# Performance work log

Measured on AMD Instinct MI355X. Metric: run time of the kernel, lower is better.

The kernel has to match this reference:

```python
import jax, jax.numpy as jnp
import numpy as np

N_NODES = 100000
N_EDGES = 1600000
IN_CH, HID, EMB = 128, 64, 32


def _glorot(key, shape):
    lim = np.sqrt(6.0 / (shape[0] + shape[1])).astype(np.float32)
    return jax.random.uniform(key, shape, jnp.float32, -lim, lim)


def setup_inputs() -> dict:
    key = jax.random.key(0)
    ks = jax.random.split(key, 5)
    x = jax.random.normal(ks[0], (N_NODES, IN_CH), dtype=jnp.float32)
    edges = jax.random.randint(ks[1], (2, N_EDGES), 0, N_NODES)
    W1 = _glorot(ks[2], (IN_CH, HID)); b1 = jnp.zeros((HID,), jnp.float32)
    W2 = _glorot(ks[3], (HID, EMB)); b2 = jnp.zeros((EMB,), jnp.float32)
    W3 = _glorot(ks[4], (HID, EMB)); b3 = jnp.zeros((EMB,), jnp.float32)
    return {"x": x, "edges": edges, "W1": W1, "b1": b1,
            "W2": W2, "b2": b2, "W3": W3, "b3": b3}


def reference(x, edges, W1, b1, W2, b2, W3, b3):
    N = x.shape[0]
    # GCNConv default: add self-loops, symmetric D^-1/2 A D^-1/2 normalization
    loop = jnp.arange(N, dtype=edges.dtype)
    src = jnp.concatenate([edges[0], loop])  # [E+N] message sources
    dst = jnp.concatenate([edges[1], loop])  # [E+N] message targets
    deg = jax.ops.segment_sum(jnp.ones_like(dst, dtype=x.dtype), dst, num_segments=N)
    dinv = jnp.where(deg > 0, jax.lax.rsqrt(deg), 0.0)
    norm = dinv[src] * dinv[dst]  # [E+N], cached across the three convs (cached=True)

    def gcn(h, W, b):
        h = h @ W                                  # [N, out]
        msg = h[src] * norm[:, None]               # gather + edge scale
        return jax.ops.segment_sum(msg, dst, num_segments=N) + b  # scatter-add

    h = jax.nn.relu(gcn(x, W1, b1))
    return gcn(h, W2, b2), gcn(h, W3, b3)
```

## Files before the change

### kernel.cpp

```cpp
#include <hip/hip_runtime.h>

#define NN 100000
#define NE 1600000
#define NB 391
#define CHUNK 4096
#define NCHUNK 391

typedef __attribute__((ext_vector_type(8))) short short8_t;
typedef __attribute__((ext_vector_type(4))) float float4_t;

__device__ inline unsigned short f2bf(float f) {
    unsigned int u = __float_as_uint(f);
    unsigned int r = u + 0x7fffu + ((u >> 16) & 1u);
    return (unsigned short)(r >> 16);
}
__device__ inline float bf_lo(unsigned int u) { return __uint_as_float(u << 16); }
__device__ inline float bf_hi(unsigned int u) { return __uint_as_float(u & 0xffff0000u); }

__global__ __launch_bounds__(256) void k_pre(const float* __restrict__ W1,
                                             unsigned short* __restrict__ wtb,
                                             int* __restrict__ bhist) {
    int f = blockIdx.x * 256 + threadIdx.x;
    int c = f >> 7, k = f & 127;
    wtb[f] = f2bf(W1[k * 64 + c]);
    if (f < NB) bhist[f] = 0;
}

__global__ __launch_bounds__(256) void k_hist(const int* __restrict__ dst,
                                              int* __restrict__ bhist) {
    __shared__ int lh[NB];
    int t = threadIdx.x;
    for (int i = t; i < NB; i += 256) lh[i] = 0;
    __syncthreads();
    for (int e = blockIdx.x * 256 + t; e < NE; e += 256 * 256)
        atomicAdd(&lh[dst[e] >> 8], 1);
    __syncthreads();
    for (int i = t; i < NB; i += 256)
        if (lh[i]) atomicAdd(&bhist[i], lh[i]);
}

__global__ __launch_bounds__(256) void k_scanb(const int* __restrict__ bhist,
                                               int* __restrict__ boff,
                                               int* __restrict__ bcur) {
    __shared__ int sh[256];
    int t = threadIdx.x;
    int base = t * 2;
    int v0 = (base + 0 < NB) ? bhist[base + 0] : 0;
    int v1 = (base + 1 < NB) ? bhist[base + 1] : 0;
    int tsum = v0 + v1;
    sh[t] = tsum;
    __syncthreads();
    for (int d = 1; d < 256; d <<= 1) {
        int x = (t >= d) ? sh[t - d] : 0;
        __syncthreads();
        sh[t] += x;
        __syncthreads();
    }
    int excl = sh[t] - tsum;
    if (base + 0 < NB) { boff[base + 0] = excl;      bcur[base + 0] = excl; }
    if (base + 1 < NB) { boff[base + 1] = excl + v0; bcur[base + 1] = excl + v0; }
    if (t == 255) boff[NB] = sh[255];
}

__global__ __launch_bounds__(512) void k_fuse(const float* __restrict__ x,
                                              const unsigned short* __restrict__ wtb,
                                              unsigned short* __restrict__ t1b,
                                              const int* __restrict__ src,
                                              const int* __restrict__ dst,
                                              int* __restrict__ bcur,
                                              unsigned int* __restrict__ pairs) {
    __shared__ __align__(16) unsigned char smem[52224];
    const int b = blockIdx.x;
    const int t = threadIdx.x;

    if ((b % 3) == 2) {
        int* lh    = (int*)smem;
        int* lbase = lh + NB;
        int e0 = (b / 3) * CHUNK;
        int e1 = min(e0 + CHUNK, NE);
        for (int i = t; i < NB; i += 512) lh[i] = 0;
        __syncthreads();
        for (int e = e0 + t; e < e1; e += 512)
            atomicAdd(&lh[dst[e] >> 8], 1);
        __syncthreads();
        int rot = (int)(((unsigned)(b / 3) * 97u) % NB);
        for (int i = t; i < NB; i += 512) {
            int ii = i + rot; if (ii >= NB) ii -= NB;
            int h = lh[ii];
            lbase[ii] = h ? atomicAdd(&bcur[ii], h) : 0;
        }
        __syncthreads();
        for (int i = t; i < NB; i += 512) lh[i] = 0;
        __syncthreads();
        for (int e = e0 + t; e < e1; e += 512) {
            int d = dst[e];
            int bk = d >> 8;
            int r = atomicAdd(&lh[bk], 1);
            pairs[lbase[bk] + r] = (unsigned int)src[e] | ((unsigned int)(d & 255) << 17);
        }
    } else {
        unsigned short* lx = (unsigned short*)smem;
        unsigned short* lw = (unsigned short*)(smem + 34816);
        const int tile = 2 * (b / 3) + (b % 3);
        const int row0 = tile * 128;
        const int nrows = min(128, NN - row0);

        #pragma unroll
        for (int i = 0; i < 8; ++i) {
            int f = t + i * 512;
            int r = f >> 5, c4 = f & 31;
            float4 v = make_float4(0.f, 0.f, 0.f, 0.f);
            if (r < nrows) v = ((const float4*)(x + (size_t)(row0 + r) * 128))[c4];
            ushort4 o;
            o.x = f2bf(v.x); o.y = f2bf(v.y); o.z = f2bf(v.z); o.w = f2bf(v.w);
            *(ushort4*)&lx[r * 136 + c4 * 4] = o;
        }
        #pragma unroll
        for (int i = 0; i < 2; ++i) {
            int f = t + i * 512;
            int c = f >> 4, c8 = f & 15;
            uint4 v = ((const uint4*)wtb)[f];
            *(uint4*)&lw[c * 136 + c8 * 8] = v;
        }
        __syncthreads();

        const int w = t >> 6, l = t & 63;
        const int m15 = l & 15, kg = l >> 4;
        const unsigned short* pa = &lx[(w * 16 + m15) * 136 + kg * 8];
        const unsigned short* pb = &lw[m15 * 136 + kg * 8];

        float4_t acc[4];
        #pragma unroll
        for (int cb = 0; cb < 4; ++cb) acc[cb] = (float4_t){0.f, 0.f, 0.f, 0.f};

        #pragma unroll
        for (int ks = 0; ks < 4; ++ks) {
            short8_t a = *(const short8_t*)(pa + ks * 32);
            #pragma unroll
            for (int cb = 0; cb < 4; ++cb) {
                short8_t bb = *(const short8_t*)(pb + cb * (16 * 136) + ks * 32);
                acc[cb] = __builtin_amdgcn_mfma_f32_16x16x32_bf16(a, bb, acc[cb], 0, 0, 0);
            }
        }

        #pragma unroll
        for (int r = 0; r < 4; ++r) {
            int lrow = w * 16 + kg * 4 + r;
            if (lrow < nrows) {
                size_t grow = (size_t)(row0 + lrow);
                #pragma unroll
                for (int cb = 0; cb < 4; ++cb)
                    t1b[grow * 64 + cb * 16 + m15] = f2bf(acc[cb][r]);
            }
        }
    }
}

__global__ __launch_bounds__(256) void k_fine(const unsigned int* __restrict__ pairs,
                                              const int* __restrict__ boff,
                                              int* __restrict__ csr_off,
                                              int* __restrict__ csr_src,
                                              float* __restrict__ dinv) {
    __shared__ int lcnt[256];
    __shared__ int sc[256];
    __shared__ int lofs[256];
    int t = threadIdx.x;
    int b = blockIdx.x;
    int n0 = b << 8;
    int nnode = min(256, NN - n0);
    int bO = boff[b], bE = boff[b + 1];

    lcnt[t] = 0;
    __syncthreads();
    for (int e = bO + t; e < bE; e += 256)
        atomicAdd(&lcnt[pairs[e] >> 17], 1);
    __syncthreads();
    sc[t] = lcnt[t];
    __syncthreads();
    for (int d = 1; d < 256; d <<= 1) {
        int x = (t >= d) ? sc[t - d] : 0;
        __syncthreads();
        sc[t] += x;
        __syncthreads();
    }
    {
        int excl = sc[t] - lcnt[t];
        lofs[t] = excl;
        if (t < nnode) {
            int n = n0 + t;
            csr_off[n] = bO + excl;
            dinv[n] = rsqrtf(1.0f + (float)lcnt[t]);
        }
        lcnt[t] = 0;
    }
    if (b == NB - 1 && t == 0) csr_off[NN] = NE;
    __syncthreads();
    for (int e = bO + t; e < bE; e += 256) {
        unsigned int w = pairs[e];
        int li = (int)(w >> 17);
        int r = atomicAdd(&lcnt[li], 1);
        csr_src[bO + lofs[li] + r] = (int)(w & 0x1FFFFu);
    }
}

__global__ __launch_bounds__(256) void k_gather8(const int* __restrict__ off,
                                                 const int* __restrict__ csr,
                                                 const float* __restrict__ dinv,
                                                 const unsigned short* __restrict__ hb,
                                                 const float* __restrict__ bias,
                                                 unsigned int* __restrict__ outp) {
    int idx = blockIdx.x * 256 + threadIdx.x;
    int n = idx >> 3;
    if (n >= NN) return;
    int c8 = idx & 7;
    const uint4* h4 = (const uint4*)hb;
    float dn = dinv[n];
    float a0[8], a1[8];
    {
        uint4 v = h4[(size_t)n * 8 + c8];
        a0[0] = dn * bf_lo(v.x); a0[1] = dn * bf_hi(v.x);
        a0[2] = dn * bf_lo(v.y); a0[3] = dn * bf_hi(v.y);
        a0[4] = dn * bf_lo(v.z); a0[5] = dn * bf_hi(v.z);
        a0[6] = dn * bf_lo(v.w); a0[7] = dn * bf_hi(v.w);
        #pragma unroll
        for (int j = 0; j < 8; ++j) a1[j] = 0.f;
    }
    int b = off[n], e = off[n + 1];
    int i = b;
    for (; i + 1 < e; i += 2) {
        int s0 = csr[i], s1 = csr[i + 1];
        float w0 = dinv[s0], w1 = dinv[s1];
        uint4 v0 = h4[(size_t)s0 * 8 + c8];
        uint4 v1 = h4[(size_t)s1 * 8 + c8];
        a0[0] += w0 * bf_lo(v0.x); a0[1] += w0 * bf_hi(v0.x);
        a0[2] += w0 * bf_lo(v0.y); a0[3] += w0 * bf_hi(v0.y);
        a0[4] += w0 * bf_lo(v0.z); a0[5] += w0 * bf_hi(v0.z);
        a0[6] += w0 * bf_lo(v0.w); a0[7] += w0 * bf_hi(v0.w);
        a1[0] += w1 * bf_lo(v1.x); a1[1] += w1 * bf_hi(v1.x);
        a1[2] += w1 * bf_lo(v1.y); a1[3] += w1 * bf_hi(v1.y);
        a1[4] += w1 * bf_lo(v1.z); a1[5] += w1 * bf_hi(v1.z);
        a1[6] += w1 * bf_lo(v1.w); a1[7] += w1 * bf_hi(v1.w);
    }
    if (i < e) {
        int s = csr[i];
        float w = dinv[s];
        uint4 v = h4[(size_t)s * 8 + c8];
        a0[0] += w * bf_lo(v.x); a0[1] += w * bf_hi(v.x);
        a0[2] += w * bf_lo(v.y); a0[3] += w * bf_hi(v.y);
        a0[4] += w * bf_lo(v.z); a0[5] += w * bf_hi(v.z);
        a0[6] += w * bf_lo(v.w); a0[7] += w * bf_hi(v.w);
    }
    float4 b0 = ((const float4*)bias)[c8 * 2];
    float4 b1v = ((const float4*)bias)[c8 * 2 + 1];
    float o[8];
    o[0] = dn * fmaxf(dn * (a0[0] + a1[0]) + b0.x, 0.f);
    o[1] = dn * fmaxf(dn * (a0[1] + a1[1]) + b0.y, 0.f);
    o[2] = dn * fmaxf(dn * (a0[2] + a1[2]) + b0.z, 0.f);
    o[3] = dn * fmaxf(dn * (a0[3] + a1[3]) + b0.w, 0.f);
    o[4] = dn * fmaxf(dn * (a0[4] + a1[4]) + b1v.x, 0.f);
    o[5] = dn * fmaxf(dn * (a0[5] + a1[5]) + b1v.y, 0.f);
    o[6] = dn * fmaxf(dn * (a0[6] + a1[6]) + b1v.z, 0.f);
    o[7] = dn * fmaxf(dn * (a0[7] + a1[7]) + b1v.w, 0.f);
    uint4 p;
    p.x = (unsigned int)f2bf(o[0]) | ((unsigned int)f2bf(o[1]) << 16);
    p.y = (unsigned int)f2bf(o[2]) | ((unsigned int)f2bf(o[3]) << 16);
    p.z = (unsigned int)f2bf(o[4]) | ((unsigned int)f2bf(o[5]) << 16);
    p.w = (unsigned int)f2bf(o[6]) | ((unsigned int)f2bf(o[7]) << 16);
    ((uint4*)outp)[(size_t)n * 8 + c8] = p;
}

__global__ __launch_bounds__(256) void k_gg2(const int* __restrict__ off,
                                             const int* __restrict__ csr,
                                             const float* __restrict__ dinv,
                                             const unsigned short* __restrict__ hb,
                                             const float* __restrict__ W2, const float* __restrict__ b2,
                                             const float* __restrict__ W3, const float* __restrict__ b3,
                                             float* __restrict__ out) {
    __shared__ float as_[32][72];
    __shared__ float wc[64 * 64];
    __shared__ float bc[64];
    const int t = threadIdx.x;
    const int row0 = blockIdx.x * 32;

    #pragma unroll
    for (int i = 0; i < 16; ++i) {
        int f = t + i * 256;
        int k = f >> 6, c = f & 63;
        wc[f] = (c < 32) ? W2[k * 32 + c] : W3[k * 32 + (c - 32)];
    }
    if (t < 64) bc[t] = (t < 32) ? b2[t] : b3[t - 32];

    {
        const int nl = t >> 3;
        const int n = row0 + nl;
        const int c8 = t & 7;
        const uint4* h4 = (const uint4*)hb;
        float dn = dinv[n];
        float acc[8];
        uint4 v = h4[(size_t)n * 8 + c8];
        acc[0] = bf_lo(v.x); acc[1] = bf_hi(v.x);
        acc[2] = bf_lo(v.y); acc[3] = bf_hi(v.y);
        acc[4] = bf_lo(v.z); acc[5] = bf_hi(v.z);
        acc[6] = bf_lo(v.w); acc[7] = bf_hi(v.w);
        int b = off[n], e = off[n + 1];
        for (int i = b; i < e; ++i) {
            int s = csr[i];
            uint4 u = h4[(size_t)s * 8 + c8];
            acc[0] += bf_lo(u.x); acc[1] += bf_hi(u.x);
            acc[2] += bf_lo(u.y); acc[3] += bf_hi(u.y);
            acc[4] += bf_lo(u.z); acc[5] += bf_hi(u.z);
            acc[6] += bf_lo(u.w); acc[7] += bf_hi(u.w);
        }
        float* dp = &as_[nl][c8 * 8];
        #pragma unroll
        for (int j = 0; j < 8; ++j) dp[j] = dn * acc[j];
    }
    __syncthreads();

    const int tc = t & 15;
    const int tr = t >> 4;
    float acc[2][4];
    #pragma unroll
    for (int i = 0; i < 2; ++i)
        #pragma unroll
        for (int j = 0; j < 4; ++j) acc[i][j] = 0.f;

    #pragma unroll 4
    for (int k = 0; k < 64; ++k) {
        float4 wv = *(const float4*)&wc[k * 64 + tc * 4];
        #pragma unroll
        for (int i = 0; i < 2; ++i) {
            float xv = as_[tr * 2 + i][k];
            acc[i][0] += xv * wv.x; acc[i][1] += xv * wv.y;
            acc[i][2] += xv * wv.z; acc[i][3] += xv * wv.w;
        }
    }
    const int c0 = tc * 4;
    float4 bias = *(float4*)&bc[c0];
    #pragma unroll
    for (int i = 0; i < 2; ++i) {
        int r = tr * 2 + i;
        float4 o = make_float4(acc[i][0] + bias.x, acc[i][1] + bias.y,
                               acc[i][2] + bias.z, acc[i][3] + bias.w);
        size_t row = (size_t)(row0 + r);
        float* p = (tc < 8) ? (out + row * 32 + c0)
                            : (out + (size_t)NN * 32 + row * 32 + (c0 - 32));
        *(float4*)p = o;
    }
}

extern "C" void kernel_launch(void* const* d_in, const int* in_sizes, int n_in,
                              void* d_out, int out_size, void* d_ws, size_t ws_size,
                              hipStream_t stream) {
    const float* x  = (const float*)d_in[0];
    const int* edges = (const int*)d_in[1];
    const float* W1 = (const float*)d_in[2];
    const float* b1 = (const float*)d_in[3];
    const float* W2 = (const float*)d_in[4];
    const float* b2 = (const float*)d_in[5];
    const float* W3 = (const float*)d_in[6];
    const float* b3 = (const float*)d_in[7];
    float* out = (float*)d_out;

    const int* srcs = edges;
    const int* dsts = edges + NE;

    int*   csr_off = (int*)d_ws;
    float* dinv    = (float*)((int*)d_ws + 100004);
    int*   csr_src = (int*)d_ws + 200004;
    int*   bhist   = (int*)d_ws + 1800004;
    int*   boff    = (int*)d_ws + 1800396;
    int*   bcur    = (int*)d_ws + 1800788;
    unsigned short* wtb = (unsigned short*)((int*)d_ws + 1801184);
    unsigned short* t1b = (unsigned short*)((int*)d_ws + 1805280);
    unsigned int*   pairs = (unsigned int*)((int*)d_ws + 5005280);
    unsigned short* h1b   = (unsigned short*)pairs;

    dim3 blk(256);
    const int gN8 = (NN * 8 + 255) / 256;
    const int gT2 = NN / 32;

    k_pre<<<32, blk, 0, stream>>>(W1, wtb, bhist);
    k_hist<<<256, blk, 0, stream>>>(dsts, bhist);
    k_scanb<<<1, blk, 0, stream>>>(bhist, boff, bcur);

    k_fuse<<<3 * NCHUNK, dim3(512), 0, stream>>>(x, wtb, t1b, srcs, dsts, bcur, pairs);

    k_fine<<<NB, blk, 0, stream>>>(pairs, boff, csr_off, csr_src, dinv);

    k_gather8<<<gN8, blk, 0, stream>>>(csr_off, csr_src, dinv, t1b, b1,
                                       (unsigned int*)h1b);
    k_gg2<<<gT2, blk, 0, stream>>>(csr_off, csr_src, dinv, h1b, W2, b2, W3, b3, out);
}
```

Baseline: 163.2 us.

## Transform before aggregating in layer two with MFMA GEMM then gather

Replaces the fused gather-then-matmul second layer with a bf16 MFMA GEMM that projects h1 into a combined 64-wide W2|W3 output, followed by a separate CSR gather over the projected features that applies normalization and bias. This reorders aggregation and projection, moves the small matmul onto matrix cores, and lets the gather loop process two neighbors per iteration. It adds an extra kernel launch and a bf16 rounding of the projected features, and it stages the bf16 weights in the tail of the output buffer before that buffer is overwritten.

```diff
diff --git a/kernel.cpp b/kernel.cpp
--- a/kernel.cpp
+++ b/kernel.cpp
@@ -18,11 +18,19 @@
 __device__ inline float bf_hi(unsigned int u) { return __uint_as_float(u & 0xffff0000u); }
 
 __global__ __launch_bounds__(256) void k_pre(const float* __restrict__ W1,
+                                             const float* __restrict__ W2,
+                                             const float* __restrict__ W3,
                                              unsigned short* __restrict__ wtb,
+                                             unsigned short* __restrict__ wt2,
                                              int* __restrict__ bhist) {
     int f = blockIdx.x * 256 + threadIdx.x;
     int c = f >> 7, k = f & 127;
     wtb[f] = f2bf(W1[k * 64 + c]);
+    if (f < 4096) {
+        int c2 = f >> 6, k2 = f & 63;
+        float v = (c2 < 32) ? W2[k2 * 32 + c2] : W3[k2 * 32 + (c2 - 32)];
+        wt2[f] = f2bf(v);
+    }
     if (f < NB) bhist[f] = 0;
 }
 
@@ -269,84 +277,121 @@
     ((uint4*)outp)[(size_t)n * 8 + c8] = p;
 }
 
-__global__ __launch_bounds__(256) void k_gg2(const int* __restrict__ off,
-                                             const int* __restrict__ csr,
-                                             const float* __restrict__ dinv,
-                                             const unsigned short* __restrict__ hb,
-                                             const float* __restrict__ W2, const float* __restrict__ b2,
-                                             const float* __restrict__ W3, const float* __restrict__ b3,
-                                             float* __restrict__ out) {
-    __shared__ float as_[32][72];
-    __shared__ float wc[64 * 64];
-    __shared__ float bc[64];
+__global__ __launch_bounds__(512) void k_gemm23(const unsigned short* __restrict__ h1b,
+                                                const unsigned short* __restrict__ wt2,
+                                                unsigned short* __restrict__ y) {
+    __shared__ __align__(16) unsigned short lx[128 * 72];
+    __shared__ __align__(16) unsigned short lw[64 * 72];
     const int t = threadIdx.x;
-    const int row0 = blockIdx.x * 32;
-
-    #pragma unroll
-    for (int i = 0; i < 16; ++i) {
-        int f = t + i * 256;
-        int k = f >> 6, c = f & 63;
-        wc[f] = (c < 32) ? W2[k * 32 + c] : W3[k * 32 + (c - 32)];
-    }
-    if (t < 64) bc[t] = (t < 32) ? b2[t] : b3[t - 32];
-
-    {
-        const int nl = t >> 3;
-        const int n = row0 + nl;
-        const int c8 = t & 7;
-        const uint4* h4 = (const uint4*)hb;
-        float dn = dinv[n];
-        float acc[8];
-        uint4 v = h4[(size_t)n * 8 + c8];
-        acc[0] = bf_lo(v.x); acc[1] = bf_hi(v.x);
-        acc[2] = bf_lo(v.y); acc[3] = bf_hi(v.y);
-        acc[4] = bf_lo(v.z); acc[5] = bf_hi(v.z);
-        acc[6] = bf_lo(v.w); acc[7] = bf_hi(v.w);
-        int b = off[n], e = off[n + 1];
-        for (int i = b; i < e; ++i) {
-            int s = csr[i];
-            uint4 u = h4[(size_t)s * 8 + c8];
-            acc[0] += bf_lo(u.x); acc[1] += bf_hi(u.x);
-            acc[2] += bf_lo(u.y); acc[3] += bf_hi(u.y);
-            acc[4] += bf_lo(u.z); acc[5] += bf_hi(u.z);
-            acc[6] += bf_lo(u.w); acc[7] += bf_hi(u.w);
-        }
-        float* dp = &as_[nl][c8 * 8];
-        #pragma unroll
-        for (int j = 0; j < 8; ++j) dp[j] = dn * acc[j];
-    }
-    __syncthreads();
-
-    const int tc = t & 15;
-    const int tr = t >> 4;
-    float acc[2][4];
-    #pragma unroll
-    for (int i = 0; i < 2; ++i)
-        #pragma unroll
-        for (int j = 0; j < 4; ++j) acc[i][j] = 0.f;
-
-    #pragma unroll 4
-    for (int k = 0; k < 64; ++k) {
-        float4 wv = *(const float4*)&wc[k * 64 + tc * 4];
-        #pragma unroll
-        for (int i = 0; i < 2; ++i) {
-            float xv = as_[tr * 2 + i][k];
-            acc[i][0] += xv * wv.x; acc[i][1] += xv * wv.y;
-            acc[i][2] += xv * wv.z; acc[i][3] += xv * wv.w;
-        }
-    }
-    const int c0 = tc * 4;
-    float4 bias = *(float4*)&bc[c0];
+    const int row0 = blockIdx.x * 128;
+    const int nrows = min(128, NN - row0);
+
     #pragma unroll
     for (int i = 0; i < 2; ++i) {
-        int r = tr * 2 + i;
-        float4 o = make_float4(acc[i][0] + bias.x, acc[i][1] + bias.y,
-                               acc[i][2] + bias.z, acc[i][3] + bias.w);
-        size_t row = (size_t)(row0 + r);
-        float* p = (tc < 8) ? (out + row * 32 + c0)
-                            : (out + (size_t)NN * 32 + row * 32 + (c0 - 32));
-        *(float4*)p = o;
-    }
+        int f = t + i * 512;
+        int r = f >> 3, c8 = f & 7;
+        uint4 v = make_uint4(0u, 0u, 0u, 0u);
+        if (r < nrows) v = ((const uint4*)h1b)[(size_t)(row0 + r) * 8 + c8];
+        *(uint4*)&lx[r * 72 + c8 * 8] = v;
+    }
+    if (t < 512) {
+        int c = t >> 3, c8 = t & 7;
+        uint4 v = ((const uint4*)wt2)[t];
+        *(uint4*)&lw[c * 72 + c8 * 8] = v;
+    }
+    __syncthreads();
+
+    const int w = t >> 6, l = t & 63;
+    const int m15 = l & 15, kg = l >> 4;
+    const unsigned short* pa = &lx[(w * 16 + m15) * 72 + kg * 8];
+    const unsigned short* pb = &lw[m15 * 72 + kg * 8];
+
+    float4_t acc[4];
+    #pragma unroll
+    for (int cb = 0; cb < 4; ++cb) acc[cb] = (float4_t){0.f, 0.f, 0.f, 0.f};
+
+    #pragma unroll
+    for (int ks = 0; ks < 2; ++ks) {
+        short8_t a = *(const short8_t*)(pa + ks * 32);
+        #pragma unroll
+        for (int cb = 0; cb < 4; ++cb) {
+            short8_t bb = *(const short8_t*)(pb + cb * (16 * 72) + ks * 32);
+            acc[cb] = __builtin_amdgcn_mfma_f32_16x16x32_bf16(a, bb, acc[cb], 0, 0, 0);
+        }
+    }
+
+    #pragma unroll
+    for (int r = 0; r < 4; ++r) {
+        int lrow = w * 16 + kg * 4 + r;
+        if (lrow < nrows) {
+            size_t grow = (size_t)(row0 + lrow);
+            #pragma unroll
+            for (int cb = 0; cb < 4; ++cb)
+                y[grow * 64 + cb * 16 + m15] = f2bf(acc[cb][r]);
+        }
+    }
+}
+
+__global__ __launch_bounds__(256) void k_gatherO(const int* __restrict__ off,
+                                                 const int* __restrict__ csr,
+                                                 const float* __restrict__ dinv,
+                                                 const unsigned short* __restrict__ yb,
+                                                 const float* __restrict__ b2,
+                                                 const float* __restrict__ b3,
+                                                 float* __restrict__ out) {
+    int idx = blockIdx.x * 256 + threadIdx.x;
+    int n = idx >> 3;
+    int c8 = idx & 7;
+    const uint4* h4 = (const uint4*)yb;
+    float a0[8], a1[8];
+    {
+        uint4 v = h4[(size_t)n * 8 + c8];
+        a0[0] = bf_lo(v.x); a0[1] = bf_hi(v.x);
+        a0[2] = bf_lo(v.y); a0[3] = bf_hi(v.y);
+        a0[4] = bf_lo(v.z); a0[5] = bf_hi(v.z);
+        a0[6] = bf_lo(v.w); a0[7] = bf_hi(v.w);
+        #pragma unroll
+        for (int j = 0; j < 8; ++j) a1[j] = 0.f;
+    }
+    int b = off[n], e = off[n + 1];
+    int i = b;
+    for (; i + 1 < e; i += 2) {
+        int s0 = csr[i], s1 = csr[i + 1];
+        uint4 v0 = h4[(size_t)s0 * 8 + c8];
+        uint4 v1 = h4[(size_t)s1 * 8 + c8];
+        a0[0] += bf_lo(v0.x); a0[1] += bf_hi(v0.x);
+        a0[2] += bf_lo(v0.y); a0[3] += bf_hi(v0.y);
+        a0[4] += bf_lo(v0.z); a0[5] += bf_hi(v0.z);
+        a0[6] += bf_lo(v0.w); a0[7] += bf_hi(v0.w);
+        a1[0] += bf_lo(v1.x); a1[1] += bf_hi(v1.x);
+        a1[2] += bf_lo(v1.y); a1[3] += bf_hi(v1.y);
+        a1[4] += bf_lo(v1.z); a1[5] += bf_hi(v1.z);
+        a1[6] += bf_lo(v1.w); a1[7] += bf_hi(v1.w);
+    }
+    if (i < e) {
+        uint4 v = h4[(size_t)csr[i] * 8 + c8];
+        a0[0] += bf_lo(v.x); a0[1] += bf_hi(v.x);
+        a0[2] += bf_lo(v.y); a0[3] += bf_hi(v.y);
+        a0[4] += bf_lo(v.z); a0[5] += bf_hi(v.z);
+        a0[6] += bf_lo(v.w); a0[7] += bf_hi(v.w);
+    }
+    float dn = dinv[n];
+    const float* bp = (c8 < 4) ? (b2 + c8 * 8) : (b3 + (c8 - 4) * 8);
+    float4 q0 = *(const float4*)bp;
+    float4 q1 = *(const float4*)(bp + 4);
+    float4 o0, o1;
+    o0.x = dn * (a0[0] + a1[0]) + q0.x;
+    o0.y = dn * (a0[1] + a1[1]) + q0.y;
+    o0.z = dn * (a0[2] + a1[2]) + q0.z;
+    o0.w = dn * (a0[3] + a1[3]) + q0.w;
+    o1.x = dn * (a0[4] + a1[4]) + q1.x;
+    o1.y = dn * (a0[5] + a1[5]) + q1.y;
+    o1.z = dn * (a0[6] + a1[6]) + q1.z;
+    o1.w = dn * (a0[7] + a1[7]) + q1.w;
+    float* op = (c8 < 4) ? (out + (size_t)n * 32 + c8 * 8)
+                         : (out + (size_t)NN * 32 + (size_t)n * 32 + (c8 - 4) * 8);
+    *(float4*)op = o0;
+    *(float4*)(op + 4) = o1;
 }
 
 extern "C" void kernel_launch(void* const* d_in, const int* in_sizes, int n_in,
@@ -373,14 +418,16 @@
     int*   bcur    = (int*)d_ws + 1800788;
     unsigned short* wtb = (unsigned short*)((int*)d_ws + 1801184);
     unsigned short* t1b = (unsigned short*)((int*)d_ws + 1805280);
+    unsigned short* y   = t1b;
     unsigned int*   pairs = (unsigned int*)((int*)d_ws + 5005280);
     unsigned short* h1b   = (unsigned short*)pairs;
+    unsigned short* wt2 = (unsigned short*)(out + 6400000 - 2048);
 
     dim3 blk(256);
     const int gN8 = (NN * 8 + 255) / 256;
-    const int gT2 = NN / 32;
-
-    k_pre<<<32, blk, 0, stream>>>(W1, wtb, bhist);
+    const int gT23 = (NN + 127) / 128;
+
+    k_pre<<<32, blk, 0, stream>>>(W1, W2, W3, wtb, wt2, bhist);
     k_hist<<<256, blk, 0, stream>>>(dsts, bhist);
     k_scanb<<<1, blk, 0, stream>>>(bhist, boff, bcur);
 
@@ -390,5 +437,6 @@
 
     k_gather8<<<gN8, blk, 0, stream>>>(csr_off, csr_src, dinv, t1b, b1,
                                        (unsigned int*)h1b);
-    k_gg2<<<gT2, blk, 0, stream>>>(csr_off, csr_src, dinv, h1b, W2, b2, W3, b3, out);
-}
+    k_gemm23<<<gT23, dim3(512), 0, stream>>>(h1b, wt2, y);
+    k_gatherO<<<gN8, blk, 0, stream>>>(csr_off, csr_src, dinv, y, b2, b3, out);
+}
```

New measurement: 149.8 us. 8.2% less time.
